# Kernel optimization log

Measured on AMD Instinct MI355X. Metric: run time of the kernel, lower is better.

The kernel has to match this reference:

```python
import jax, jax.numpy as jnp
import numpy as np

K_FRAC = 0.7  # fraction of highest-loss samples kept

def setup_inputs() -> dict:
    key = jax.random.key(0)
    k1, k2 = jax.random.split(key)
    N, C = 8192, 32000
    inp = jax.random.normal(k1, (N, C), dtype=jnp.float32)
    target = jax.random.randint(k2, (N,), 0, C, dtype=jnp.int64)
    return {"input": inp, "target": target}

def reference(input, target):
    N = input.shape[0]
    # per-sample NLL of log-softmax: loss_i = -log_softmax(input)_i[target_i]
    logp = jax.nn.log_softmax(input, axis=1)  # [N, C]
    per_sample = -jnp.take_along_axis(logp, target[:, None], axis=1)[:, 0]  # [N]
    k_count = int(K_FRAC * N)  # static, matches int(self.k * N)
    if K_FRAC == 1.0:
        valid = per_sample
    else:
        valid, _ = jax.lax.top_k(per_sample, k_count)  # top-k largest losses
    return jnp.mean(valid)
```

## Files before the change

### kernel.cpp

```cpp
#include <hip/hip_runtime.h>
#include <math.h>

#define NROWS 8192
#define NCOLS 32000
#define NF4   (NCOLS / 4)
#define KSEL  5734
#define RPB   4
#define NBLK  (NROWS / RPB)

typedef float f32x4 __attribute__((ext_vector_type(4)));

__device__ __forceinline__ float exp4(f32x4 v) {
    return (__expf(v.x) + __expf(v.y)) + (__expf(v.z) + __expf(v.w));
}

__global__ __launch_bounds__(256) void row_nll_kernel(
    const float* __restrict__ inp, const int* __restrict__ tgt,
    float* __restrict__ losses)
{
    const int tid  = threadIdx.x;
    const int row0 = blockIdx.x * RPB;
    __shared__ float ss[4];

    for (int r = 0; r < RPB; ++r) {
        const int row = row0 + r;
        const f32x4* __restrict__ rp = (const f32x4*)(inp + (size_t)row * NCOLS);

        float s0 = 0.f, s1 = 0.f, s2 = 0.f, s3 = 0.f;
        float s4 = 0.f, s5 = 0.f, s6 = 0.f, s7 = 0.f;

        int j = tid;
#pragma unroll 1
        for (int t = 0; t < 3; ++t, j += 2048) {
            f32x4 a = __builtin_nontemporal_load(rp + j);
            f32x4 b = __builtin_nontemporal_load(rp + j + 256);
            f32x4 c = __builtin_nontemporal_load(rp + j + 512);
            f32x4 d = __builtin_nontemporal_load(rp + j + 768);
            f32x4 e = __builtin_nontemporal_load(rp + j + 1024);
            f32x4 f = __builtin_nontemporal_load(rp + j + 1280);
            f32x4 g = __builtin_nontemporal_load(rp + j + 1536);
            f32x4 h = __builtin_nontemporal_load(rp + j + 1792);
            s0 += exp4(a); s1 += exp4(b); s2 += exp4(c); s3 += exp4(d);
            s4 += exp4(e); s5 += exp4(f); s6 += exp4(g); s7 += exp4(h);
        }
        {
            f32x4 a = __builtin_nontemporal_load(rp + j);
            f32x4 b = __builtin_nontemporal_load(rp + j + 256);
            f32x4 c = __builtin_nontemporal_load(rp + j + 512);
            f32x4 d = __builtin_nontemporal_load(rp + j + 768);
            f32x4 e = __builtin_nontemporal_load(rp + j + 1024);
            f32x4 f = __builtin_nontemporal_load(rp + j + 1280);
            f32x4 g = __builtin_nontemporal_load(rp + j + 1536);
            s0 += exp4(a); s1 += exp4(b); s2 += exp4(c); s3 += exp4(d);
            s4 += exp4(e); s5 += exp4(f); s6 += exp4(g);
            if (tid < 64) {
                f32x4 z = __builtin_nontemporal_load(rp + 7936 + tid);
                s7 += exp4(z);
            }
        }

        float s = ((s0 + s1) + (s2 + s3)) + ((s4 + s5) + (s6 + s7));

        for (int off = 32; off > 0; off >>= 1) s += __shfl_down(s, off);

        if ((tid & 63) == 0) ss[tid >> 6] = s;
        __syncthreads();
        if (tid == 0) {
            float S = (ss[0] + ss[1]) + (ss[2] + ss[3]);
            float xt = inp[(size_t)row * NCOLS + tgt[row]];
            losses[row] = __logf(S) - xt;
        }
        __syncthreads();
    }
}

__global__ __launch_bounds__(256) void topk_mean_kernel(
    const float* __restrict__ losses, float* __restrict__ out)
{
    const int tid = threadIdx.x;
    __shared__ int red_i[4];
    __shared__ float red_f[4];
    __shared__ unsigned int s_prefix;
    __shared__ int s_kk;

    unsigned int key[32];
#pragma unroll
    for (int i = 0; i < 32; i++)
        key[i] = __float_as_uint(losses[tid + i * 256]);

    if (tid == 0) { s_prefix = 0u; s_kk = KSEL; }
    __syncthreads();

    for (int bit = 31; bit >= 0; bit--) {
        const unsigned int cand = s_prefix | (1u << bit);
        const unsigned int mask = ~((1u << bit) - 1u);
        int c = 0;
#pragma unroll
        for (int i = 0; i < 32; i++) c += (int)((key[i] & mask) == cand);
        for (int off = 32; off > 0; off >>= 1) c += __shfl_down(c, off);
        if ((tid & 63) == 0) red_i[tid >> 6] = c;
        __syncthreads();
        if (tid == 0) {
            int tot = (red_i[0] + red_i[1]) + (red_i[2] + red_i[3]);
            if (tot >= s_kk) s_prefix = cand; else s_kk -= tot;
        }
        __syncthreads();
    }

    const unsigned int pivot = s_prefix;
    float sum = 0.0f;
    int cnt = 0;
#pragma unroll
    for (int i = 0; i < 32; i++) {
        if (key[i] > pivot) { sum += __uint_as_float(key[i]); cnt++; }
    }
    for (int off = 32; off > 0; off >>= 1) {
        sum += __shfl_down(sum, off);
        cnt += __shfl_down(cnt, off);
    }
    if ((tid & 63) == 0) { red_f[tid >> 6] = sum; red_i[tid >> 6] = cnt; }
    __syncthreads();
    if (tid == 0) {
        float ts = (red_f[0] + red_f[1]) + (red_f[2] + red_f[3]);
        int tc = (red_i[0] + red_i[1]) + (red_i[2] + red_i[3]);
        float pv = __uint_as_float(pivot);
        out[0] = (ts + (float)(KSEL - tc) * pv) / (float)KSEL;
    }
}

extern "C" void kernel_launch(void* const* d_in, const int* in_sizes, int n_in,
                              void* d_out, int out_size, void* d_ws, size_t ws_size,
                              hipStream_t stream) {
    const float* inp = (const float*)d_in[0];
    const int*   tgt = (const int*)d_in[1];
    float* losses = (float*)d_ws;

    row_nll_kernel<<<NBLK, 256, 0, stream>>>(inp, tgt, losses);
    topk_mean_kernel<<<1, 256, 0, stream>>>(losses, (float*)d_out);
}
```

Baseline: 1.256 ms.

## Assign one wavefront per row to drop block-level barriers in NLL kernel

Each 64-lane wavefront now processes a whole row independently, replacing the earlier scheme where all 256 threads cooperated on each of four rows in sequence. Rows are reduced with wave shuffles only, which removes the shared-memory exchange and the two __syncthreads per row. The tradeoff is fewer threads in flight per row, so each wave issues more sequential loads (15 unrolled iterations plus a tail), and memory-level parallelism per row may drop.

Result: no change. 1.257 ms (+0.1%).

```diff
diff --git a/kernel.cpp b/kernel.cpp
--- a/kernel.cpp
+++ b/kernel.cpp
@@ -5,8 +5,7 @@
 #define NCOLS 32000
 #define NF4   (NCOLS / 4)
 #define KSEL  5734
-#define RPB   4
-#define NBLK  (NROWS / RPB)
+#define NBLK  (NROWS / 4)
 
 typedef float f32x4 __attribute__((ext_vector_type(4)));
 
@@ -18,59 +17,45 @@
     const float* __restrict__ inp, const int* __restrict__ tgt,
     float* __restrict__ losses)
 {
-    const int tid  = threadIdx.x;
-    const int row0 = blockIdx.x * RPB;
-    __shared__ float ss[4];
+    const int lane = threadIdx.x & 63;
+    const int wid  = threadIdx.x >> 6;
+    const int row  = blockIdx.x * 4 + wid;
+    const f32x4* __restrict__ rp = (const f32x4*)(inp + (size_t)row * NCOLS);
 
-    for (int r = 0; r < RPB; ++r) {
-        const int row = row0 + r;
-        const f32x4* __restrict__ rp = (const f32x4*)(inp + (size_t)row * NCOLS);
+    float s0 = 0.f, s1 = 0.f, s2 = 0.f, s3 = 0.f;
+    float s4 = 0.f, s5 = 0.f, s6 = 0.f, s7 = 0.f;
 
-        float s0 = 0.f, s1 = 0.f, s2 = 0.f, s3 = 0.f;
-        float s4 = 0.f, s5 = 0.f, s6 = 0.f, s7 = 0.f;
+    int j = lane;
+#pragma unroll 1
+    for (int t = 0; t < 15; ++t, j += 512) {
+        f32x4 a = __builtin_nontemporal_load(rp + j);
+        f32x4 b = __builtin_nontemporal_load(rp + j + 64);
+        f32x4 c = __builtin_nontemporal_load(rp + j + 128);
+        f32x4 d = __builtin_nontemporal_load(rp + j + 192);
+        f32x4 e = __builtin_nontemporal_load(rp + j + 256);
+        f32x4 f = __builtin_nontemporal_load(rp + j + 320);
+        f32x4 g = __builtin_nontemporal_load(rp + j + 384);
+        f32x4 h = __builtin_nontemporal_load(rp + j + 448);
+        s0 += exp4(a); s1 += exp4(b); s2 += exp4(c); s3 += exp4(d);
+        s4 += exp4(e); s5 += exp4(f); s6 += exp4(g); s7 += exp4(h);
+    }
+    {
+        f32x4 a = __builtin_nontemporal_load(rp + j);
+        f32x4 b = __builtin_nontemporal_load(rp + j + 64);
+        f32x4 c = __builtin_nontemporal_load(rp + j + 128);
+        f32x4 d = __builtin_nontemporal_load(rp + j + 192);
+        f32x4 e = __builtin_nontemporal_load(rp + j + 256);
+        s0 += exp4(a); s1 += exp4(b); s2 += exp4(c);
+        s3 += exp4(d); s4 += exp4(e);
+    }
 
-        int j = tid;
-#pragma unroll 1
-        for (int t = 0; t < 3; ++t, j += 2048) {
-            f32x4 a = __builtin_nontemporal_load(rp + j);
-            f32x4 b = __builtin_nontemporal_load(rp + j + 256);
-            f32x4 c = __builtin_nontemporal_load(rp + j + 512);
-            f32x4 d = __builtin_nontemporal_load(rp + j + 768);
-            f32x4 e = __builtin_nontemporal_load(rp + j + 1024);
-            f32x4 f = __builtin_nontemporal_load(rp + j + 1280);
-            f32x4 g = __builtin_nontemporal_load(rp + j + 1536);
-            f32x4 h = __builtin_nontemporal_load(rp + j + 1792);
-            s0 += exp4(a); s1 += exp4(b); s2 += exp4(c); s3 += exp4(d);
-            s4 += exp4(e); s5 += exp4(f); s6 += exp4(g); s7 += exp4(h);
-        }
-        {
-            f32x4 a = __builtin_nontemporal_load(rp + j);
-            f32x4 b = __builtin_nontemporal_load(rp + j + 256);
-            f32x4 c = __builtin_nontemporal_load(rp + j + 512);
-            f32x4 d = __builtin_nontemporal_load(rp + j + 768);
-            f32x4 e = __builtin_nontemporal_load(rp + j + 1024);
-            f32x4 f = __builtin_nontemporal_load(rp + j + 1280);
-            f32x4 g = __builtin_nontemporal_load(rp + j + 1536);
-            s0 += exp4(a); s1 += exp4(b); s2 += exp4(c); s3 += exp4(d);
-            s4 += exp4(e); s5 += exp4(f); s6 += exp4(g);
-            if (tid < 64) {
-                f32x4 z = __builtin_nontemporal_load(rp + 7936 + tid);
-                s7 += exp4(z);
-            }
-        }
+    float s = ((s0 + s1) + (s2 + s3)) + ((s4 + s5) + (s6 + s7));
 
-        float s = ((s0 + s1) + (s2 + s3)) + ((s4 + s5) + (s6 + s7));
+    for (int off = 32; off > 0; off >>= 1) s += __shfl_down(s, off);
 
-        for (int off = 32; off > 0; off >>= 1) s += __shfl_down(s, off);
-
-        if ((tid & 63) == 0) ss[tid >> 6] = s;
-        __syncthreads();
-        if (tid == 0) {
-            float S = (ss[0] + ss[1]) + (ss[2] + ss[3]);
-            float xt = inp[(size_t)row * NCOLS + tgt[row]];
-            losses[row] = __logf(S) - xt;
-        }
-        __syncthreads();
+    if (lane == 0) {
+        float xt = inp[(size_t)row * NCOLS + tgt[row]];
+        losses[row] = __logf(s) - xt;
     }
 }
 
```
